# Kernel tuning notes

Hardware: AMD Instinct MI355X
Metric: run time of the kernel (lower is better)

The kernel has to match this reference:

```python
import jax, jax.numpy as jnp
import numpy as np

B, T, D = 2, 2048, 1024
H, DH = 16, 64
WINDOW = 256
SCALE = DH ** -0.5


def setup_inputs() -> dict:
    key = jax.random.key(0)
    ks = jax.random.split(key, 5)
    x = jax.random.normal(ks[0], (B, T, D), dtype=jnp.float32)
    # Linear params (y = x @ W + b form)
    w_qkv = jax.random.normal(ks[1], (D, 3 * D), dtype=jnp.float32) * (D ** -0.5)
    b_qkv = jnp.zeros((3 * D,), dtype=jnp.float32)
    w_out = jax.random.normal(ks[2], (D, D), dtype=jnp.float32) * (D ** -0.5)
    b_out = jnp.zeros((D,), dtype=jnp.float32)
    return {"x": x, "w_qkv": w_qkv, "b_qkv": b_qkv, "w_out": w_out, "b_out": b_out}


def reference(x, w_qkv, b_qkv, w_out, b_out):
    Bs, Ts, Ds = x.shape
    qkv = x @ w_qkv + b_qkv  # [B,T,3D]
    q, k, v = jnp.split(qkv, 3, axis=-1)
    # [B,H,T,dh]
    def heads(t):
        return t.reshape(Bs, Ts, H, DH).transpose(0, 2, 1, 3)
    q, k, v = heads(q), heads(k), heads(v)
    scores = jnp.einsum('bhqd,bhkd->bhqk', q, k) * SCALE
    i = jnp.arange(Ts)[:, None]
    j = jnp.arange(Ts)[None, :]
    # allowed: i - WINDOW <= j <= i  (causal + local window)
    allowed = (j <= i) & (j >= i - WINDOW)
    scores = jnp.where(allowed, scores, -jnp.inf)
    attn = jax.nn.softmax(scores, axis=-1)  # dropout is identity in eval
    out = jnp.einsum('bhqk,bhkd->bhqd', attn, v)
    out = out.transpose(0, 2, 1, 3).reshape(Bs, Ts, Ds)
    return out @ w_out + b_out
```

## Files before the change

### kernel.cpp

```cpp
#include <hip/hip_runtime.h>

#define BN 2
#define T_DIM 2048
#define D_DIM 1024
#define H_N 16
#define DH_N 64
#define WIN 256
#define NROWS (BN * T_DIM)
#define KDIM 1024

typedef __attribute__((ext_vector_type(8))) short bf16x8;
typedef __attribute__((ext_vector_type(4))) float f32x4;
typedef __attribute__((ext_vector_type(8))) unsigned short ushort8;
typedef __attribute__((ext_vector_type(4))) unsigned short u16x4;

static __device__ __forceinline__ unsigned short f2bf(float f) {
  unsigned int u = __float_as_uint(f);
  unsigned int r = (u + 0x7FFFu + ((u >> 16) & 1u)) >> 16;
  return (unsigned short)r;
}

static __device__ __forceinline__ void gl_lds16(const void* g, void* l) {
  __builtin_amdgcn_global_load_lds(
      (const __attribute__((address_space(1))) unsigned int*)g,
      (__attribute__((address_space(3))) unsigned int*)l, 16, 0, 0);
}

__global__ __launch_bounds__(256) void convert_bf(const float* __restrict__ src,
                                                  unsigned short* __restrict__ dst) {
  int i = (blockIdx.x * 256 + threadIdx.x) * 8;
  float4 a = *(const float4*)(src + i);
  float4 b = *(const float4*)(src + i + 4);
  ushort8 o;
  o[0] = f2bf(a.x); o[1] = f2bf(a.y); o[2] = f2bf(a.z); o[3] = f2bf(a.w);
  o[4] = f2bf(b.x); o[5] = f2bf(b.y); o[6] = f2bf(b.z); o[7] = f2bf(b.w);
  *(ushort8*)(dst + i) = o;
}

__global__ __launch_bounds__(256) void convert_t(const float* __restrict__ src,
                                                 unsigned short* __restrict__ dst,
                                                 int R, int C) {
  __shared__ float tile[64][65];
  const int t = threadIdx.x;
  const int bc = blockIdx.x * 64, br = blockIdx.y * 64;
#pragma unroll
  for (int i = 0; i < 16; ++i) {
    int idx = i * 256 + t;
    int r = idx >> 6, c = idx & 63;
    tile[r][c] = src[(size_t)(br + r) * C + bc + c];
  }
  __syncthreads();
#pragma unroll
  for (int i = 0; i < 16; ++i) {
    int idx = i * 256 + t;
    int r = idx >> 6, c = idx & 63;
    dst[(size_t)(bc + r) * R + br + c] = f2bf(tile[c][r]);
  }
}

template <int EPI>
__global__ __launch_bounds__(256) void mfma_gemm(
    const unsigned short* __restrict__ A, const unsigned short* __restrict__ Bt,
    const float* __restrict__ bias, float* __restrict__ fo,
    unsigned short* __restrict__ qo, unsigned short* __restrict__ ko,
    unsigned short* __restrict__ vto) {
  __shared__ unsigned short As[128 * 32];
  __shared__ unsigned short Bs[128 * 32];
  const int tid = threadIdx.x;
  const int w = tid >> 6, l = tid & 63;
  const int wr = w >> 1, wc = w & 1;
  const int r0 = blockIdx.y * 128, c0 = blockIdx.x * 128;

  f32x4 acc[4][4];
#pragma unroll
  for (int i = 0; i < 4; ++i)
#pragma unroll
    for (int j = 0; j < 4; ++j) acc[i][j] = (f32x4){0.f, 0.f, 0.f, 0.f};

  const unsigned short* Ag = A + (size_t)r0 * KDIM;
  const unsigned short* Bg = Bt + (size_t)c0 * KDIM;
  const int srow = l >> 2;
  const int skoff = (l & 3) * 8;

  for (int k0 = 0; k0 < KDIM; k0 += 32) {
#pragma unroll
    for (int i = 0; i < 2; ++i) {
      int chunk = i * 4 + w;
      int mrow = chunk * 16 + srow;
      gl_lds16(Ag + (size_t)mrow * KDIM + k0 + skoff, (char*)As + chunk * 1024);
      gl_lds16(Bg + (size_t)mrow * KDIM + k0 + skoff, (char*)Bs + chunk * 1024);
    }
    __syncthreads();

    bf16x8 a[4], b[4];
#pragma unroll
    for (int mi = 0; mi < 4; ++mi)
      a[mi] = *(const bf16x8*)((const char*)As +
                               (wr * 64 + mi * 16 + (l & 15)) * 64 + (l >> 4) * 16);
#pragma unroll
    for (int ni = 0; ni < 4; ++ni)
      b[ni] = *(const bf16x8*)((const char*)Bs +
                               (wc * 64 + ni * 16 + (l & 15)) * 64 + (l >> 4) * 16);
#pragma unroll
    for (int mi = 0; mi < 4; ++mi)
#pragma unroll
      for (int ni = 0; ni < 4; ++ni)
        acc[mi][ni] = __builtin_amdgcn_mfma_f32_16x16x32_bf16(a[mi], b[ni],
                                                              acc[mi][ni], 0, 0, 0);
    __syncthreads();
  }

#pragma unroll
  for (int mi = 0; mi < 4; ++mi) {
#pragma unroll
    for (int ni = 0; ni < 4; ++ni) {
      int row = r0 + wr * 64 + mi * 16 + (l >> 4) * 4;
      int col = c0 + wc * 64 + ni * 16 + (l & 15);
      float bv = bias[col];
      if (EPI == 0) {
#pragma unroll
        for (int j = 0; j < 4; ++j)
          fo[(size_t)(row + j) * D_DIM + col] = acc[mi][ni][j] + bv;
      } else {
        int which = col >> 10;
        int h = (col >> 6) & 15;
        int dh = col & 63;
        int b_ = row >> 11, t = row & 2047;
        if (which == 2) {
          u16x4 pk;
#pragma unroll
          for (int j = 0; j < 4; ++j) pk[j] = f2bf(acc[mi][ni][j] + bv);
          *(u16x4*)(vto + ((size_t)(b_ * H_N + h) * DH_N + dh) * T_DIM + t) = pk;
        } else {
          float mul = (which == 0) ? 0.125f : 1.0f;
          unsigned short* dst = (which == 0) ? qo : ko;
#pragma unroll
          for (int j = 0; j < 4; ++j)
            dst[((size_t)(b_ * H_N + h) * T_DIM + t + j) * DH_N + dh] =
                f2bf((acc[mi][ni][j] + bv) * mul);
        }
      }
    }
  }
}

__global__ __launch_bounds__(256) void attn_mfma(
    const unsigned short* __restrict__ qbf,
    const unsigned short* __restrict__ kbf,
    const unsigned short* __restrict__ vtbf,
    unsigned short* __restrict__ ctx) {
  __shared__ unsigned short Ks[64 * 64];
  __shared__ unsigned short Vs[64 * 64];
  const int tid = threadIdx.x;
  const int w = tid >> 6, l = tid & 63;
  const int g = l >> 4, ln = l & 15;
  const int qt = blockIdx.x & 31;
  const int bh = blockIdx.x >> 5;
  const int q0 = qt * 64;
  const int q_abs = q0 + w * 16 + ln;

  const unsigned short* kp = kbf + (size_t)bh * T_DIM * DH_N;
  const unsigned short* vtp = vtbf + (size_t)bh * DH_N * T_DIM;

  bf16x8 qf0, qf1;
  {
    const unsigned short* qp = qbf + ((size_t)bh * T_DIM + q_abs) * DH_N;
    qf0 = *(const bf16x8*)(qp + g * 8);
    qf1 = *(const bf16x8*)(qp + 32 + g * 8);
  }

  f32x4 acc_o[4];
#pragma unroll
  for (int nd = 0; nd < 4; ++nd) acc_o[nd] = (f32x4){0.f, 0.f, 0.f, 0.f};
  float m = -1e30f, lsum = 0.f;

  const int kt_lo = (q0 >= WIN) ? (q0 - WIN) : 0;
  for (int kt = kt_lo; kt <= q0; kt += 64) {
    __syncthreads();
#pragma unroll
    for (int i = 0; i < 2; ++i) {
      int chunk = i * 256 + tid;
      int row = chunk >> 3, c16 = chunk & 7;
      int sc16 = c16 ^ (row & 7);
      int kap = 32 * ((row >> 4) & 1) + 8 * ((row & 15) >> 2) + 4 * (row >> 5) +
                (row & 3);
      gl_lds16(kp + (size_t)(kt + kap) * DH_N + sc16 * 8, (char*)Ks + chunk * 16);
      gl_lds16(vtp + (size_t)row * T_DIM + kt + sc16 * 8, (char*)Vs + chunk * 16);
    }
    __syncthreads();

    f32x4 sacc[4];
#pragma unroll
    for (int nk = 0; nk < 4; ++nk) sacc[nk] = (f32x4){0.f, 0.f, 0.f, 0.f};
#pragma unroll
    for (int ks = 0; ks < 2; ++ks) {
      bf16x8 qf = ks ? qf1 : qf0;
#pragma unroll
      for (int nk = 0; nk < 4; ++nk) {
        int rrow = nk * 16 + ln;
        int c16 = ks * 4 + g;
        bf16x8 kf = *(const bf16x8*)((const char*)Ks + rrow * 128 +
                                     ((c16 ^ (rrow & 7)) * 16));
        sacc[nk] = __builtin_amdgcn_mfma_f32_16x16x32_bf16(kf, qf, sacc[nk], 0, 0, 0);
      }
    }

    float p[4][4];
    float tm = -1e30f;
#pragma unroll
    for (int nk = 0; nk < 4; ++nk)
#pragma unroll
      for (int j = 0; j < 4; ++j) {
        int k_abs = kt + 32 * (nk & 1) + 8 * g + 4 * (nk >> 1) + j;
        float s = sacc[nk][j];
        bool ok = (k_abs <= q_abs) && (k_abs + WIN >= q_abs);
        s = ok ? s : -1e30f;
        p[nk][j] = s;
        tm = fmaxf(tm, s);
      }
    tm = fmaxf(tm, __shfl_xor(tm, 16, 64));
    tm = fmaxf(tm, __shfl_xor(tm, 32, 64));
    float mn = fmaxf(m, tm);
    float sc = __expf(m - mn);
    float ps = 0.f;
#pragma unroll
    for (int nk = 0; nk < 4; ++nk)
#pragma unroll
      for (int j = 0; j < 4; ++j) {
        p[nk][j] = __expf(p[nk][j] - mn);
        ps += p[nk][j];
      }
    ps += __shfl_xor(ps, 16, 64);
    ps += __shfl_xor(ps, 32, 64);
    lsum = lsum * sc + ps;
    m = mn;
#pragma unroll
    for (int nd = 0; nd < 4; ++nd) {
      acc_o[nd][0] *= sc; acc_o[nd][1] *= sc;
      acc_o[nd][2] *= sc; acc_o[nd][3] *= sc;
    }

    unsigned int pk[4][2];
#pragma unroll
    for (int nk = 0; nk < 4; ++nk) {
      pk[nk][0] = (unsigned)f2bf(p[nk][0]) | ((unsigned)f2bf(p[nk][1]) << 16);
      pk[nk][1] = (unsigned)f2bf(p[nk][2]) | ((unsigned)f2bf(p[nk][3]) << 16);
    }

#pragma unroll
    for (int ks = 0; ks < 2; ++ks) {
      union { unsigned int d[4]; bf16x8 v; } pf;
      pf.d[0] = pk[ks][0];     pf.d[1] = pk[ks][1];
      pf.d[2] = pk[2 + ks][0]; pf.d[3] = pk[2 + ks][1];
#pragma unroll
      for (int nd = 0; nd < 4; ++nd) {
        int drow = nd * 16 + ln;
        int c16 = ks * 4 + g;
        bf16x8 vf = *(const bf16x8*)((const char*)Vs + drow * 128 +
                                     ((c16 ^ (drow & 7)) * 16));
        acc_o[nd] = __builtin_amdgcn_mfma_f32_16x16x32_bf16(vf, pf.v, acc_o[nd],
                                                            0, 0, 0);
      }
    }
  }

  float inv = 1.f / lsum;
  const int b_ = bh >> 4, h = bh & 15;
  unsigned short* op = ctx + ((size_t)b_ * T_DIM + q_abs) * D_DIM + h * DH_N;
#pragma unroll
  for (int nd = 0; nd < 4; ++nd) {
    u16x4 o;
#pragma unroll
    for (int j = 0; j < 4; ++j) o[j] = f2bf(acc_o[nd][j] * inv);
    *(u16x4*)(op + nd * 16 + g * 4) = o;
  }
}

extern "C" void kernel_launch(void* const* d_in, const int* in_sizes, int n_in,
                              void* d_out, int out_size, void* d_ws,
                              size_t ws_size, hipStream_t stream) {
  const float* x = (const float*)d_in[0];
  const float* w_qkv = (const float*)d_in[1];
  const float* b_qkv = (const float*)d_in[2];
  const float* w_out = (const float*)d_in[3];
  const float* b_out = (const float*)d_in[4];
  float* out = (float*)d_out;

  const size_t per = (size_t)BN * H_N * T_DIM * DH_N;
  unsigned short* qbf = (unsigned short*)d_ws;
  unsigned short* kbf = qbf + per;
  unsigned short* vtbf = kbf + per;
  unsigned short* xbf = vtbf + per;
  unsigned short* wqkvt = xbf + (size_t)NROWS * D_DIM;
  unsigned short* woutt = wqkvt + (size_t)3 * D_DIM * D_DIM;
  unsigned short* ctxbf = woutt + (size_t)D_DIM * D_DIM;

  convert_bf<<<dim3(NROWS * D_DIM / (256 * 8)), dim3(256), 0, stream>>>(x, xbf);
  convert_t<<<dim3(3 * D_DIM / 64, D_DIM / 64), dim3(256), 0, stream>>>(
      w_qkv, wqkvt, D_DIM, 3 * D_DIM);
  convert_t<<<dim3(D_DIM / 64, D_DIM / 64), dim3(256), 0, stream>>>(
      w_out, woutt, D_DIM, D_DIM);

  mfma_gemm<1><<<dim3(3 * D_DIM / 128, NROWS / 128), dim3(256), 0, stream>>>(
      xbf, wqkvt, b_qkv, nullptr, qbf, kbf, vtbf);

  attn_mfma<<<dim3(BN * H_N * (T_DIM / 64)), dim3(256), 0, stream>>>(
      qbf, kbf, vtbf, ctxbf);

  mfma_gemm<0><<<dim3(D_DIM / 128, NROWS / 128), dim3(256), 0, stream>>>(
      ctxbf, woutt, b_out, out, nullptr, nullptr, nullptr);
}
```

Before: 108.0 us.

## Replace QKV GEMM with 256x256 double-buffered, swizzled, XCD-remapped kernel

The QKV projection now uses a dedicated 512-thread kernel with 256x256 output tiles. It double-buffers LDS stages loaded via global_load_lds and XOR-swizzles LDS slots to avoid bank conflicts. It remaps block IDs so neighbouring tiles land on the same XCD, and raises wave priority around the MFMA bursts. The aim is more data reuse per LDS byte and overlap of loads with compute; in exchange only 192 blocks are launched (fewer than the CU count) and register pressure is higher.

```diff
diff --git a/kernel.cpp b/kernel.cpp
--- a/kernel.cpp
+++ b/kernel.cpp
@@ -58,12 +58,128 @@
   }
 }
 
-template <int EPI>
-__global__ __launch_bounds__(256) void mfma_gemm(
+__global__ __launch_bounds__(512) void gemm256_qkv(
     const unsigned short* __restrict__ A, const unsigned short* __restrict__ Bt,
-    const float* __restrict__ bias, float* __restrict__ fo,
-    unsigned short* __restrict__ qo, unsigned short* __restrict__ ko,
-    unsigned short* __restrict__ vto) {
+    const float* __restrict__ bias, unsigned short* __restrict__ qo,
+    unsigned short* __restrict__ ko, unsigned short* __restrict__ vto) {
+  __shared__ unsigned short As[2][8192];
+  __shared__ unsigned short Bs[2][8192];
+
+  const int tid = threadIdx.x;
+  const int w = tid >> 6, l = tid & 63;
+  const int wr = w >> 2, wc = w & 3;
+
+  const int id = blockIdx.x;
+  const int wg = (id & 7) * 24 + (id >> 3);
+  const int bx = wg % 12, by = wg / 12;
+  const int r0 = by * 256, c0 = bx * 256;
+
+  const unsigned short* Ag = A + (size_t)r0 * KDIM;
+  const unsigned short* Bg = Bt + (size_t)c0 * KDIM;
+
+  f32x4 acc[8][4];
+#pragma unroll
+  for (int i = 0; i < 8; ++i)
+#pragma unroll
+    for (int j = 0; j < 4; ++j) acc[i][j] = (f32x4){0.f, 0.f, 0.f, 0.f};
+
+  const int srow_lo = l >> 2;
+  const int srcslot = (l & 3) ^ ((l >> 2) & 3);
+
+#define STAGE(kt, bsel)                                                        \
+  do {                                                                         \
+    const int k0_ = (kt) * 32;                                                 \
+    _Pragma("unroll") for (int i_ = 0; i_ < 2; ++i_) {                         \
+      int sb_ = i_ * 8 + w;                    \
+      int row_ = sb_ * 16 + srow_lo;                                           \
+      gl_lds16(Ag + (size_t)row_ * KDIM + k0_ + srcslot * 8,                   \
+               (char*)&As[bsel][0] + sb_ * 1024);                              \
+      gl_lds16(Bg + (size_t)row_ * KDIM + k0_ + srcslot * 8,                   \
+               (char*)&Bs[bsel][0] + sb_ * 1024);                              \
+    }                                                                          \
+  } while (0)
+
+  const int kslc = l >> 4;
+
+  STAGE(0, 0);
+  asm volatile("s_waitcnt vmcnt(0)" ::: "memory");
+  __builtin_amdgcn_s_barrier();
+
+  for (int t = 0; t < 32; ++t) {
+    const int cb = t & 1, nb = cb ^ 1;
+    if (t + 1 < 32) STAGE(t + 1, nb);
+
+    bf16x8 a[4], b[4];
+#pragma unroll
+    for (int mi = 0; mi < 4; ++mi) {
+      int row = wr * 128 + mi * 16 + (l & 15);
+      a[mi] = *(const bf16x8*)((const char*)&As[cb][0] + row * 64 +
+                               ((kslc ^ (row & 3)) << 4));
+    }
+#pragma unroll
+    for (int ni = 0; ni < 4; ++ni) {
+      int row = wc * 64 + ni * 16 + (l & 15);
+      b[ni] = *(const bf16x8*)((const char*)&Bs[cb][0] + row * 64 +
+                               ((kslc ^ (row & 3)) << 4));
+    }
+    __builtin_amdgcn_s_setprio(1);
+#pragma unroll
+    for (int mi = 0; mi < 4; ++mi)
+#pragma unroll
+      for (int ni = 0; ni < 4; ++ni)
+        acc[mi][ni] = __builtin_amdgcn_mfma_f32_16x16x32_bf16(a[mi], b[ni],
+                                                              acc[mi][ni], 0, 0, 0);
+    __builtin_amdgcn_s_setprio(0);
+#pragma unroll
+    for (int mi = 0; mi < 4; ++mi) {
+      int row = wr * 128 + (mi + 4) * 16 + (l & 15);
+      a[mi] = *(const bf16x8*)((const char*)&As[cb][0] + row * 64 +
+                               ((kslc ^ (row & 3)) << 4));
+    }
+    __builtin_amdgcn_s_setprio(1);
+#pragma unroll
+    for (int mi = 0; mi < 4; ++mi)
+#pragma unroll
+      for (int ni = 0; ni < 4; ++ni)
+        acc[mi + 4][ni] = __builtin_amdgcn_mfma_f32_16x16x32_bf16(
+            a[mi], b[ni], acc[mi + 4][ni], 0, 0, 0);
+    __builtin_amdgcn_s_setprio(0);
+
+    if (t + 1 < 32) asm volatile("s_waitcnt vmcnt(0)" ::: "memory");
+    __builtin_amdgcn_s_barrier();
+  }
+#undef STAGE
+
+  const int which = (c0 + wc * 64) >> 10;
+  const int h = ((c0 + wc * 64) >> 6) & 15;
+#pragma unroll
+  for (int mi = 0; mi < 8; ++mi) {
+#pragma unroll
+    for (int ni = 0; ni < 4; ++ni) {
+      int row = r0 + wr * 128 + mi * 16 + (l >> 4) * 4;
+      int dh = ni * 16 + (l & 15);
+      float bv = bias[c0 + wc * 64 + dh];
+      int b_ = row >> 11, t0 = row & 2047;
+      if (which == 2) {
+        u16x4 pk;
+#pragma unroll
+        for (int j = 0; j < 4; ++j) pk[j] = f2bf(acc[mi][ni][j] + bv);
+        *(u16x4*)(vto + ((size_t)(b_ * H_N + h) * DH_N + dh) * T_DIM + t0) = pk;
+      } else {
+        float mul = (which == 0) ? 0.125f : 1.0f;
+        unsigned short* dst = (which == 0) ? qo : ko;
+#pragma unroll
+        for (int j = 0; j < 4; ++j)
+          dst[((size_t)(b_ * H_N + h) * T_DIM + t0 + j) * DH_N + dh] =
+              f2bf((acc[mi][ni][j] + bv) * mul);
+      }
+    }
+  }
+}
+
+__global__ __launch_bounds__(256) void mfma_gemm_out(
+    const unsigned short* __restrict__ A, const unsigned short* __restrict__ Bt,
+    const float* __restrict__ bias, float* __restrict__ fo) {
   __shared__ unsigned short As[128 * 32];
   __shared__ unsigned short Bs[128 * 32];
   const int tid = threadIdx.x;
@@ -117,29 +233,9 @@
       int row = r0 + wr * 64 + mi * 16 + (l >> 4) * 4;
       int col = c0 + wc * 64 + ni * 16 + (l & 15);
       float bv = bias[col];
-      if (EPI == 0) {
-#pragma unroll
-        for (int j = 0; j < 4; ++j)
-          fo[(size_t)(row + j) * D_DIM + col] = acc[mi][ni][j] + bv;
-      } else {
-        int which = col >> 10;
-        int h = (col >> 6) & 15;
-        int dh = col & 63;
-        int b_ = row >> 11, t = row & 2047;
-        if (which == 2) {
-          u16x4 pk;
-#pragma unroll
-          for (int j = 0; j < 4; ++j) pk[j] = f2bf(acc[mi][ni][j] + bv);
-          *(u16x4*)(vto + ((size_t)(b_ * H_N + h) * DH_N + dh) * T_DIM + t) = pk;
-        } else {
-          float mul = (which == 0) ? 0.125f : 1.0f;
-          unsigned short* dst = (which == 0) ? qo : ko;
-#pragma unroll
-          for (int j = 0; j < 4; ++j)
-            dst[((size_t)(b_ * H_N + h) * T_DIM + t + j) * DH_N + dh] =
-                f2bf((acc[mi][ni][j] + bv) * mul);
-        }
-      }
+#pragma unroll
+      for (int j = 0; j < 4; ++j)
+        fo[(size_t)(row + j) * D_DIM + col] = acc[mi][ni][j] + bv;
     }
   }
 }
@@ -301,12 +397,12 @@
   convert_t<<<dim3(D_DIM / 64, D_DIM / 64), dim3(256), 0, stream>>>(
       w_out, woutt, D_DIM, D_DIM);
 
-  mfma_gemm<1><<<dim3(3 * D_DIM / 128, NROWS / 128), dim3(256), 0, stream>>>(
-      xbf, wqkvt, b_qkv, nullptr, qbf, kbf, vtbf);
+  gemm256_qkv<<<dim3(192), dim3(512), 0, stream>>>(xbf, wqkvt, b_qkv, qbf, kbf,
+                                                   vtbf);
 
   attn_mfma<<<dim3(BN * H_N * (T_DIM / 64)), dim3(256), 0, stream>>>(
       qbf, kbf, vtbf, ctxbf);
 
-  mfma_gemm<0><<<dim3(D_DIM / 128, NROWS / 128), dim3(256), 0, stream>>>(
-      ctxbf, woutt, b_out, out, nullptr, nullptr, nullptr);
-}
+  mfma_gemm_out<<<dim3(D_DIM / 128, NROWS / 128), dim3(256), 0, stream>>>(
+      ctxbf, woutt, b_out, out);
+}
```

After: 108.1 us. Within noise of the previous version (+0.1%).

## Pipeline GEMMs with 4-stage LDS ring, swizzled layout and larger QKV tiles

Applied to the files above, without the earlier changes.

Replaces the single-buffered templated GEMM with two specialized kernels. Each streams K-tiles through a 4-deep LDS ring using explicit vmcnt waits, so global loads overlap with MFMA work. LDS rows are XOR-swizzled to avoid bank conflicts, and MFMA issue priority is raised with setprio. The QKV GEMM moves to 256x192 tiles with 512 threads, giving exactly 256 blocks, and both grids are remapped for L2 locality. This costs more LDS and hand-tuned waitcnt counts that must exactly match the number of issued loads.

```diff
diff --git a/kernel.cpp b/kernel.cpp
--- a/kernel.cpp
+++ b/kernel.cpp
@@ -58,88 +58,235 @@
   }
 }
 
-template <int EPI>
-__global__ __launch_bounds__(256) void mfma_gemm(
+__global__ __launch_bounds__(512) void gemm_qkv_p4(
     const unsigned short* __restrict__ A, const unsigned short* __restrict__ Bt,
-    const float* __restrict__ bias, float* __restrict__ fo,
-    unsigned short* __restrict__ qo, unsigned short* __restrict__ ko,
-    unsigned short* __restrict__ vto) {
-  __shared__ unsigned short As[128 * 32];
-  __shared__ unsigned short Bs[128 * 32];
+    const float* __restrict__ bias, unsigned short* __restrict__ qo,
+    unsigned short* __restrict__ ko, unsigned short* __restrict__ vto) {
+  __shared__ unsigned short As[4][8192];
+  __shared__ unsigned short Bs[4][6144];
+
+  const int tid = threadIdx.x;
+  const int w = tid >> 6, l = tid & 63;
+  const int wr = w >> 2, wc = w & 3;
+  const bool wlt4 = (w < 4);
+  const int l15 = l & 15, kslc = l >> 4;
+
+  const int id = blockIdx.x;
+  const int wg = (id & 7) * 32 + (id >> 3);
+  const int bx = wg & 15, by = wg >> 4;
+  const int r0 = by * 256, c0 = bx * 192;
+
+  const unsigned short* Ag = A + (size_t)r0 * KDIM;
+  const unsigned short* Bg = Bt + (size_t)c0 * KDIM;
+
+  f32x4 acc[8][3];
+#pragma unroll
+  for (int i = 0; i < 8; ++i)
+#pragma unroll
+    for (int j = 0; j < 3; ++j) acc[i][j] = (f32x4){0.f, 0.f, 0.f, 0.f};
+
+  const int srow = l >> 2;
+  const int srcslot = (l & 3) ^ (srow & 3);
+
+#define STAGE_Q(T, BUF)                                                        \
+  do {                                                                         \
+    const size_t kk0 = (size_t)(T) * 32;                                       \
+    gl_lds16(Ag + (size_t)(w * 16 + srow) * KDIM + kk0 + srcslot * 8,          \
+             (char*)&As[BUF][0] + w * 1024);                                   \
+    gl_lds16(Ag + (size_t)(128 + w * 16 + srow) * KDIM + kk0 + srcslot * 8,    \
+             (char*)&As[BUF][0] + (8 + w) * 1024);                             \
+    gl_lds16(Bg + (size_t)(w * 16 + srow) * KDIM + kk0 + srcslot * 8,          \
+             (char*)&Bs[BUF][0] + w * 1024);                                   \
+    if (wlt4)                                                                  \
+      gl_lds16(Bg + (size_t)(128 + w * 16 + srow) * KDIM + kk0 + srcslot * 8,  \
+               (char*)&Bs[BUF][0] + (8 + w) * 1024);                           \
+  } while (0)
+
+#define QCOMPUTE(CB)                                                           \
+  do {                                                                         \
+    bf16x8 af[4], bfr[3];                                                      \
+    _Pragma("unroll") for (int mi = 0; mi < 4; ++mi) {                         \
+      int row = wr * 128 + mi * 16 + l15;                                      \
+      af[mi] = *(const bf16x8*)((const char*)&As[CB][0] + row * 64 +           \
+                                ((kslc ^ (row & 3)) << 4));                    \
+    }                                                                          \
+    _Pragma("unroll") for (int ni = 0; ni < 3; ++ni) {                         \
+      int row = wc * 48 + ni * 16 + l15;                                       \
+      bfr[ni] = *(const bf16x8*)((const char*)&Bs[CB][0] + row * 64 +          \
+                                 ((kslc ^ (row & 3)) << 4));                   \
+    }                                                                          \
+    __builtin_amdgcn_s_setprio(1);                                             \
+    _Pragma("unroll") for (int mi = 0; mi < 4; ++mi)                           \
+        _Pragma("unroll") for (int ni = 0; ni < 3; ++ni) acc[mi][ni] =         \
+            __builtin_amdgcn_mfma_f32_16x16x32_bf16(af[mi], bfr[ni],           \
+                                                    acc[mi][ni], 0, 0, 0);     \
+    __builtin_amdgcn_s_setprio(0);                                             \
+    _Pragma("unroll") for (int mi = 0; mi < 4; ++mi) {                         \
+      int row = wr * 128 + (mi + 4) * 16 + l15;                                \
+      af[mi] = *(const bf16x8*)((const char*)&As[CB][0] + row * 64 +           \
+                                ((kslc ^ (row & 3)) << 4));                    \
+    }                                                                          \
+    __builtin_amdgcn_s_setprio(1);                                             \
+    _Pragma("unroll") for (int mi = 0; mi < 4; ++mi)                           \
+        _Pragma("unroll") for (int ni = 0; ni < 3; ++ni) acc[mi + 4][ni] =     \
+            __builtin_amdgcn_mfma_f32_16x16x32_bf16(af[mi], bfr[ni],           \
+                                                    acc[mi + 4][ni], 0, 0, 0); \
+    __builtin_amdgcn_s_setprio(0);                                             \
+  } while (0)
+
+  STAGE_Q(0, 0);
+  STAGE_Q(1, 1);
+  STAGE_Q(2, 2);
+
+  for (int t = 0; t < 29; ++t) {
+    STAGE_Q(t + 3, (t + 3) & 3);
+    if (wlt4) asm volatile("s_waitcnt vmcnt(12)" ::: "memory");
+    else      asm volatile("s_waitcnt vmcnt(9)" ::: "memory");
+    __builtin_amdgcn_s_barrier();
+    QCOMPUTE(t & 3);
+    __builtin_amdgcn_s_barrier();
+  }
+  if (wlt4) asm volatile("s_waitcnt vmcnt(8)" ::: "memory");
+  else      asm volatile("s_waitcnt vmcnt(6)" ::: "memory");
+  __builtin_amdgcn_s_barrier();
+  QCOMPUTE(1);
+  __builtin_amdgcn_s_barrier();
+  if (wlt4) asm volatile("s_waitcnt vmcnt(4)" ::: "memory");
+  else      asm volatile("s_waitcnt vmcnt(3)" ::: "memory");
+  __builtin_amdgcn_s_barrier();
+  QCOMPUTE(2);
+  __builtin_amdgcn_s_barrier();
+  asm volatile("s_waitcnt vmcnt(0)" ::: "memory");
+  __builtin_amdgcn_s_barrier();
+  QCOMPUTE(3);
+#undef STAGE_Q
+#undef QCOMPUTE
+
+#pragma unroll
+  for (int ni = 0; ni < 3; ++ni) {
+    const int col0 = c0 + wc * 48 + ni * 16;
+    const int which = col0 >> 10;
+    const int h = (col0 >> 6) & 15;
+    const int dh = (col0 & 63) + l15;
+    const float bv = bias[col0 + l15];
+#pragma unroll
+    for (int mi = 0; mi < 8; ++mi) {
+      int row = r0 + wr * 128 + mi * 16 + (l >> 4) * 4;
+      int b_ = row >> 11, t0 = row & 2047;
+      if (which == 2) {
+        u16x4 pk;
+#pragma unroll
+        for (int j = 0; j < 4; ++j) pk[j] = f2bf(acc[mi][ni][j] + bv);
+        *(u16x4*)(vto + ((size_t)(b_ * H_N + h) * DH_N + dh) * T_DIM + t0) = pk;
+      } else {
+        float mul = (which == 0) ? 0.125f : 1.0f;
+        unsigned short* dst = (which == 0) ? qo : ko;
+#pragma unroll
+        for (int j = 0; j < 4; ++j)
+          dst[((size_t)(b_ * H_N + h) * T_DIM + t0 + j) * DH_N + dh] =
+              f2bf((acc[mi][ni][j] + bv) * mul);
+      }
+    }
+  }
+}
+
+__global__ __launch_bounds__(256) void gemm_out_p4(
+    const unsigned short* __restrict__ A, const unsigned short* __restrict__ Bt,
+    const float* __restrict__ bias, float* __restrict__ fo) {
+  __shared__ unsigned short As[4][4096];
+  __shared__ unsigned short Bs[4][4096];
+
   const int tid = threadIdx.x;
   const int w = tid >> 6, l = tid & 63;
   const int wr = w >> 1, wc = w & 1;
-  const int r0 = blockIdx.y * 128, c0 = blockIdx.x * 128;
-
-  f32x4 acc[4][4];
-#pragma unroll
-  for (int i = 0; i < 4; ++i)
-#pragma unroll
-    for (int j = 0; j < 4; ++j) acc[i][j] = (f32x4){0.f, 0.f, 0.f, 0.f};
+  const int l15 = l & 15, kslc = l >> 4;
+
+  const int id = blockIdx.x;
+  const int wg = (id & 7) * 32 + (id >> 3);
+  const int bx = wg & 7, by = wg >> 3;
+  const int r0 = by * 128, c0 = bx * 128;
 
   const unsigned short* Ag = A + (size_t)r0 * KDIM;
   const unsigned short* Bg = Bt + (size_t)c0 * KDIM;
+
+  f32x4 acc[4][4];
+#pragma unroll
+  for (int i = 0; i < 4; ++i)
+#pragma unroll
+    for (int j = 0; j < 4; ++j) acc[i][j] = (f32x4){0.f, 0.f, 0.f, 0.f};
+
   const int srow = l >> 2;
-  const int skoff = (l & 3) * 8;
-
-  for (int k0 = 0; k0 < KDIM; k0 += 32) {
-#pragma unroll
-    for (int i = 0; i < 2; ++i) {
-      int chunk = i * 4 + w;
-      int mrow = chunk * 16 + srow;
-      gl_lds16(Ag + (size_t)mrow * KDIM + k0 + skoff, (char*)As + chunk * 1024);
-      gl_lds16(Bg + (size_t)mrow * KDIM + k0 + skoff, (char*)Bs + chunk * 1024);
-    }
-    __syncthreads();
-
-    bf16x8 a[4], b[4];
-#pragma unroll
-    for (int mi = 0; mi < 4; ++mi)
-      a[mi] = *(const bf16x8*)((const char*)As +
-                               (wr * 64 + mi * 16 + (l & 15)) * 64 + (l >> 4) * 16);
-#pragma unroll
-    for (int ni = 0; ni < 4; ++ni)
-      b[ni] = *(const bf16x8*)((const char*)Bs +
-                               (wc * 64 + ni * 16 + (l & 15)) * 64 + (l >> 4) * 16);
-#pragma unroll
-    for (int mi = 0; mi < 4; ++mi)
-#pragma unroll
-      for (int ni = 0; ni < 4; ++ni)
-        acc[mi][ni] = __builtin_amdgcn_mfma_f32_16x16x32_bf16(a[mi], b[ni],
-                                                              acc[mi][ni], 0, 0, 0);
-    __syncthreads();
-  }
+  const int srcslot = (l & 3) ^ (srow & 3);
+
+#define STAGE_O(T, BUF)                                                        \
+  do {                                                                         \
+    const size_t kk0 = (size_t)(T) * 32;                                       \
+    gl_lds16(Ag + (size_t)(w * 16 + srow) * KDIM + kk0 + srcslot * 8,          \
+             (char*)&As[BUF][0] + w * 1024);                                   \
+    gl_lds16(Ag + (size_t)(64 + w * 16 + srow) * KDIM + kk0 + srcslot * 8,     \
+             (char*)&As[BUF][0] + (4 + w) * 1024);                             \
+    gl_lds16(Bg + (size_t)(w * 16 + srow) * KDIM + kk0 + srcslot * 8,          \
+             (char*)&Bs[BUF][0] + w * 1024);                                   \
+    gl_lds16(Bg + (size_t)(64 + w * 16 + srow) * KDIM + kk0 + srcslot * 8,     \
+             (char*)&Bs[BUF][0] + (4 + w) * 1024);                             \
+  } while (0)
+
+#define OCOMPUTE(CB)                                                           \
+  do {                                                                         \
+    bf16x8 af[4], bfr[4];                                                      \
+    _Pragma("unroll") for (int mi = 0; mi < 4; ++mi) {                         \
+      int row = wr * 64 + mi * 16 + l15;                                       \
+      af[mi] = *(const bf16x8*)((const char*)&As[CB][0] + row * 64 +           \
+                                ((kslc ^ (row & 3)) << 4));                    \
+    }                                                                          \
+    _Pragma("unroll") for (int ni = 0; ni < 4; ++ni) {                         \
+      int row = wc * 64 + ni * 16 + l15;                                       \
+      bfr[ni] = *(const bf16x8*)((const char*)&Bs[CB][0] + row * 64 +          \
+                                 ((kslc ^ (row & 3)) << 4));                   \
+    }                                                                          \
+    __builtin_amdgcn_s_setprio(1);                                             \
+    _Pragma("unroll") for (int mi = 0; mi < 4; ++mi)                           \
+        _Pragma("unroll") for (int ni = 0; ni < 4; ++ni) acc[mi][ni] =         \
+            __builtin_amdgcn_mfma_f32_16x16x32_bf16(af[mi], bfr[ni],           \
+                                                    acc[mi][ni], 0, 0, 0);     \
+    __builtin_amdgcn_s_setprio(0);                                             \
+  } while (0)
+
+  STAGE_O(0, 0);
+  STAGE_O(1, 1);
+  STAGE_O(2, 2);
+
+  for (int t = 0; t < 29; ++t) {
+    STAGE_O(t + 3, (t + 3) & 3);
+    asm volatile("s_waitcnt vmcnt(12)" ::: "memory");
+    __builtin_amdgcn_s_barrier();
+    OCOMPUTE(t & 3);
+    __builtin_amdgcn_s_barrier();
+  }
+  asm volatile("s_waitcnt vmcnt(8)" ::: "memory");
+  __builtin_amdgcn_s_barrier();
+  OCOMPUTE(1);
+  __builtin_amdgcn_s_barrier();
+  asm volatile("s_waitcnt vmcnt(4)" ::: "memory");
+  __builtin_amdgcn_s_barrier();
+  OCOMPUTE(2);
+  __builtin_amdgcn_s_barrier();
+  asm volatile("s_waitcnt vmcnt(0)" ::: "memory");
+  __builtin_amdgcn_s_barrier();
+  OCOMPUTE(3);
+#undef STAGE_O
+#undef OCOMPUTE
 
 #pragma unroll
   for (int mi = 0; mi < 4; ++mi) {
 #pragma unroll
     for (int ni = 0; ni < 4; ++ni) {
       int row = r0 + wr * 64 + mi * 16 + (l >> 4) * 4;
-      int col = c0 + wc * 64 + ni * 16 + (l & 15);
+      int col = c0 + wc * 64 + ni * 16 + l15;
       float bv = bias[col];
-      if (EPI == 0) {
-#pragma unroll
-        for (int j = 0; j < 4; ++j)
-          fo[(size_t)(row + j) * D_DIM + col] = acc[mi][ni][j] + bv;
-      } else {
-        int which = col >> 10;
-        int h = (col >> 6) & 15;
-        int dh = col & 63;
-        int b_ = row >> 11, t = row & 2047;
-        if (which == 2) {
-          u16x4 pk;
-#pragma unroll
-          for (int j = 0; j < 4; ++j) pk[j] = f2bf(acc[mi][ni][j] + bv);
-          *(u16x4*)(vto + ((size_t)(b_ * H_N + h) * DH_N + dh) * T_DIM + t) = pk;
-        } else {
-          float mul = (which == 0) ? 0.125f : 1.0f;
-          unsigned short* dst = (which == 0) ? qo : ko;
-#pragma unroll
-          for (int j = 0; j < 4; ++j)
-            dst[((size_t)(b_ * H_N + h) * T_DIM + t + j) * DH_N + dh] =
-                f2bf((acc[mi][ni][j] + bv) * mul);
-        }
-      }
+#pragma unroll
+      for (int j = 0; j < 4; ++j)
+        fo[(size_t)(row + j) * D_DIM + col] = acc[mi][ni][j] + bv;
     }
   }
 }
@@ -301,12 +448,11 @@
   convert_t<<<dim3(D_DIM / 64, D_DIM / 64), dim3(256), 0, stream>>>(
       w_out, woutt, D_DIM, D_DIM);
 
-  mfma_gemm<1><<<dim3(3 * D_DIM / 128, NROWS / 128), dim3(256), 0, stream>>>(
-      xbf, wqkvt, b_qkv, nullptr, qbf, kbf, vtbf);
+  gemm_qkv_p4<<<dim3(256), dim3(512), 0, stream>>>(xbf, wqkvt, b_qkv, qbf, kbf,
+                                                   vtbf);
 
   attn_mfma<<<dim3(BN * H_N * (T_DIM / 64)), dim3(256), 0, stream>>>(
       qbf, kbf, vtbf, ctxbf);
 
-  mfma_gemm<0><<<dim3(D_DIM / 128, NROWS / 128), dim3(256), 0, stream>>>(
-      ctxbf, woutt, b_out, out, nullptr, nullptr, nullptr);
-}
+  gemm_out_p4<<<dim3(256), dim3(256), 0, stream>>>(ctxbf, woutt, b_out, out);
+}
```

Result: faster. 103.6 us (-4.0%).
